# Kernel optimization log

Measured on AMD Instinct MI355X. Metric: run time of the kernel, lower is better.

Reference implementation:

```python
import jax, jax.numpy as jnp
import numpy as np

C_S, C_P, FEAT_DIM, NUM_BINS = 256, 128, 64, 22
MAX_DIST = 20.0
C_PAIR_PRE = 20
MAX_LEN = 2056.0


def get_index_embedding(indices, embed_size, max_len=MAX_LEN):
    # indices: (..., ) float; returns (..., embed_size) sinusoidal embedding
    K = jnp.arange(embed_size // 2, dtype=jnp.float32)
    ang = indices[..., None] * jnp.pi / (max_len ** (2.0 * K / embed_size))
    return jnp.concatenate([jnp.sin(ang), jnp.cos(ang)], axis=-1)


def rbf(D, D_min, D_max, D_count):
    # D: (...); returns (..., D_count) Gaussian RBF expansion
    D_mu = jnp.linspace(D_min, D_max, D_count)
    D_sigma = (D_max - D_min) / D_count
    return jnp.exp(-(((D[..., None] - D_mu) / D_sigma) ** 2))


def setup_inputs() -> dict:
    key = jax.random.key(0)
    ks = jax.random.split(key, 12)
    B, L = 1, 512
    total_edge = FEAT_DIM * 3 + NUM_BINS * 2 + C_PAIR_PRE  # 256
    inp = {
        "s": jax.random.normal(ks[0], (B, L, C_S), jnp.float32),
        "t": jax.random.normal(ks[1], (B, L, 3), jnp.float32),
        "sc_t": jax.random.normal(ks[2], (B, L, 3), jnp.float32),
        "pair_repr_pre": jax.random.normal(ks[3], (B, L, L, C_PAIR_PRE), jnp.float32),
        "p_mask": jnp.ones((B, L, L), jnp.float32),
        # linear_s_p: c_s -> feat_dim
        "W_sp": jax.random.normal(ks[4], (FEAT_DIM, C_S), jnp.float32) / np.sqrt(C_S),
        "b_sp": jnp.zeros((FEAT_DIM,), jnp.float32),
        # linear_relpos: feat_dim -> feat_dim
        "W_rp": jax.random.normal(ks[5], (FEAT_DIM, FEAT_DIM), jnp.float32) / np.sqrt(FEAT_DIM),
        "b_rp": jnp.zeros((FEAT_DIM,), jnp.float32),
        # edge_embedder: total_edge -> c_p -> c_p
        "W1": jax.random.normal(ks[6], (C_P, total_edge), jnp.float32) / np.sqrt(total_edge),
        "b1": jnp.zeros((C_P,), jnp.float32),
        "W2": jax.random.normal(ks[7], (C_P, C_P), jnp.float32) / np.sqrt(C_P),
        "b2": jnp.zeros((C_P,), jnp.float32),
    }
    return inp


def reference(s, t, sc_t, pair_repr_pre, p_mask, W_sp, b_sp, W_rp, b_rp, W1, b1, W2, b2):
    B, L, _ = s.shape
    # node projection then pairwise cross-concat -> (B, L, L, 2*feat_dim)
    p_i = jnp.einsum("bld,fd->blf", s, W_sp) + b_sp
    cross = jnp.concatenate([
        jnp.broadcast_to(p_i[:, :, None, :], (B, L, L, FEAT_DIM)),
        jnp.broadcast_to(p_i[:, None, :, :], (B, L, L, FEAT_DIM)),
    ], axis=-1)
    # relative-position sinusoidal embedding -> linear
    pos = jnp.arange(L, dtype=jnp.float32)[None, :]  # (1, L) broadcast over batch
    rel_pos = pos[:, :, None] - pos[:, None, :]      # (1, L, L)
    rel_pos = jnp.broadcast_to(rel_pos, (B, L, L))
    pos_emb = get_index_embedding(rel_pos, FEAT_DIM)
    relpos_feats = jnp.einsum("bijf,gf->bijg", pos_emb, W_rp) + b_rp
    # RBF distance expansions for backbone (t) and sidechain (sc_t) coords
    d_t = jnp.linalg.norm(t[:, :, None, :] - t[:, None, :, :], axis=-1)
    dist_feats = rbf(d_t, 0.0, MAX_DIST, NUM_BINS)
    d_sc = jnp.linalg.norm(sc_t[:, :, None, :] - sc_t[:, None, :, :], axis=-1)
    sc_feats = rbf(d_sc, 0.0, MAX_DIST, NUM_BINS)
    all_edge = jnp.concatenate([cross, relpos_feats, dist_feats, sc_feats, pair_repr_pre], axis=-1)
    # 2-layer MLP (dropout = 0 / eval mode)
    h = jax.nn.relu(jnp.einsum("bije,pe->bijp", all_edge, W1) + b1)
    edge_feats = jnp.einsum("bijp,qp->bijq", h, W2) + b2
    return edge_feats
```

## Files before the change

kernel.cpp:

```cpp
#include <hip/hip_runtime.h>
#include <hip/hip_bf16.h>


typedef __attribute__((ext_vector_type(8))) short v8s;
typedef __attribute__((ext_vector_type(4))) float v4f;

#define PI_F 3.14159265358979323846f

__device__ __forceinline__ unsigned short f2bu(float x) {
    __hip_bfloat16 h = __float2bfloat16(x);
    return *reinterpret_cast<unsigned short*>(&h);
}

__global__ __launch_bounds__(256) void precompute_kernel(
    const float* __restrict__ s, const float* __restrict__ W_sp,
    const float* __restrict__ b_sp, const float* __restrict__ W_rp,
    const float* __restrict__ b_rp, const float* __restrict__ W1,
    const float* __restrict__ W2,
    __hip_bfloat16* __restrict__ p_bf, __hip_bfloat16* __restrict__ relT,
    __hip_bfloat16* __restrict__ W1b, __hip_bfloat16* __restrict__ W2b)
{
    const int b = blockIdx.x;
    const int tid = threadIdx.x;
    __shared__ float lds[128 * 65 + 8 * 256];

    if (b < 64) {
        float* Wt   = lds;
        float* srow = lds + 128 * 65;
        const int row0 = b * 8;
        const int f  = tid & 63;
        const int rh = tid >> 6;
        #pragma unroll
        for (int k = 0; k < 8; k++) {
            const int idx = tid + 256 * k;
            const int r = idx >> 8, d = idx & 255;
            srow[r * 256 + d] = s[(row0 + r) * 256 + d];
        }
        float acc0 = b_sp[f];
        float acc1 = acc0;
        for (int pass = 0; pass < 2; pass++) {
            __syncthreads();
            #pragma unroll
            for (int k = 0; k < 32; k++) {
                const int idx = tid + 256 * k;
                const int fs = idx >> 7, ds = idx & 127;
                Wt[ds * 65 + fs] = W_sp[fs * 256 + pass * 128 + ds];
            }
            __syncthreads();
            #pragma unroll 4
            for (int d = 0; d < 128; d++) {
                const float w = Wt[d * 65 + f];
                acc0 += srow[rh * 256 + pass * 128 + d] * w;
                acc1 += srow[(rh + 4) * 256 + pass * 128 + d] * w;
            }
        }
        p_bf[(row0 + rh) * 64 + f]     = __float2bfloat16(acc0);
        p_bf[(row0 + rh + 4) * 64 + f] = __float2bfloat16(acc1);
    } else if (b < 320) {
        float* WrT  = lds;
        float* femb = lds + 64 * 65;
        const int r0 = (b - 64) * 4;
        #pragma unroll
        for (int k = 0; k < 16; k++) {
            const int idx = tid + 256 * k;
            const int g = idx >> 6, ff = idx & 63;
            WrT[ff * 65 + g] = W_rp[g * 64 + ff];
        }
        {
            const int r = tid >> 6, c = tid & 63;
            const float rel = (float)(r0 + r - 511);
            const int K = c & 31;
            const float freq = powf(2056.0f, (2.0f * (float)K) / 64.0f);
            const float ang = rel * PI_F / freq;
            femb[r * 64 + c] = (c < 32) ? sinf(ang) : cosf(ang);
        }
        __syncthreads();
        const int g = tid & 63, r = tid >> 6;
        float acc = b_rp[g];
        #pragma unroll
        for (int ff = 0; ff < 64; ff++) acc += femb[r * 64 + ff] * WrT[ff * 65 + g];
        relT[(r0 + r) * 64 + g] = __float2bfloat16(acc);
    } else {
        #pragma unroll
        for (int k = 0; k < 2; k++) {
            const int idx4 = (b - 320) * 512 + k * 256 + tid;
            const int e = idx4 * 4;
            const float4 v = (e < 32768) ? *(const float4*)&W1[e]
                                         : *(const float4*)&W2[e - 32768];
            __hip_bfloat16* dst = (e < 32768) ? (W1b + e) : (W2b + (e - 32768));
            dst[0] = __float2bfloat16(v.x);
            dst[1] = __float2bfloat16(v.y);
            dst[2] = __float2bfloat16(v.z);
            dst[3] = __float2bfloat16(v.w);
        }
    }
}

__global__ __launch_bounds__(256, 5) void edge_main(
    const float* __restrict__ t3, const float* __restrict__ sc3,
    const float* __restrict__ pre,
    const float* __restrict__ b1, const float* __restrict__ b2,
    const __hip_bfloat16* __restrict__ p_bf, const __hip_bfloat16* __restrict__ relT,
    const __hip_bfloat16* __restrict__ W1b, const __hip_bfloat16* __restrict__ W2b,
    float* __restrict__ out)
{
    __shared__ char smem[32768];

    const int tid = threadIdx.x;
    const int blk = blockIdx.x;
    const int i  = blk >> 3;
    const int j0 = (blk & 7) << 6;

    const int wv   = tid >> 6;
    const int lane = tid & 63;
    const int l16  = lane & 15;
    const int quad = lane >> 4;
    const int cbase = wv * 32;

    const float4 b1v0 = *(const float4*)&b1[cbase + quad * 4];
    const float4 b1v1 = *(const float4*)&b1[cbase + 16 + quad * 4];
    const float4 b2v0 = *(const float4*)&b2[cbase + quad * 4];
    const float4 b2v1 = *(const float4*)&b2[cbase + 16 + quad * 4];
    const __hip_bfloat16* w1m0 = W1b + (cbase + l16) * 256 + quad * 8;
    const __hip_bfloat16* w1m1 = w1m0 + 16 * 256;
    const __hip_bfloat16* w2m0 = W2b + (cbase + l16) * 128 + quad * 8;
    const __hip_bfloat16* w2m1 = w2m0 + 16 * 128;
    const v8s p10 = *(const v8s*)w1m0;
    const v8s p11 = *(const v8s*)w1m1;

    #pragma unroll
    for (int c = tid; c < 512; c += 256) {
        const int r  = c >> 3;
        const int ck = c & 7;
        const int px = (ck ^ (r & 7)) << 4;
        char* rowp = smem + r * 512;
        *(uint4*)(rowp + px)       = *(const uint4*)&p_bf[i * 64 + ck * 8];
        *(uint4*)(rowp + 128 + px) = *(const uint4*)&p_bf[(j0 + r) * 64 + ck * 8];
        *(uint4*)(rowp + 256 + px) = *(const uint4*)&relT[(i - (j0 + r) + 511) * 64 + ck * 8];
    }
    for (int c = tid; c < 320; c += 256) {
        const int r = c / 5;
        const int q = c % 5;
        const int col = 236 + q * 4;
        const float4 v = *(const float4*)&pre[((size_t)i * 512 + j0 + r) * 20 + q * 4];
        union { unsigned short s4[4]; uint2 u; } pk;
        pk.s4[0] = f2bu(v.x); pk.s4[1] = f2bu(v.y);
        pk.s4[2] = f2bu(v.z); pk.s4[3] = f2bu(v.w);
        const int off = r * 512 + (((col >> 3) ^ (r & 7)) << 4) + ((col & 7) * 2);
        *(uint2*)(smem + off) = pk.u;
    }
    {
        const int r  = tid >> 2;
        const int fo = (tid & 3) * 11;
        const int j = j0 + r;
        const float dxt = t3[i * 3 + 0] - t3[j * 3 + 0];
        const float dyt = t3[i * 3 + 1] - t3[j * 3 + 1];
        const float dzt = t3[i * 3 + 2] - t3[j * 3 + 2];
        const float dt = sqrtf(dxt * dxt + dyt * dyt + dzt * dzt);
        const float dxs = sc3[i * 3 + 0] - sc3[j * 3 + 0];
        const float dys = sc3[i * 3 + 1] - sc3[j * 3 + 1];
        const float dzs = sc3[i * 3 + 2] - sc3[j * 3 + 2];
        const float ds = sqrtf(dxs * dxs + dys * dys + dzs * dzs);
        char* rowp = smem + r * 512;
        const int rx = r & 7;
        #pragma unroll
        for (int q = 0; q < 11; q++) {
            const int f = fo + q;
            const float d = (f < 22) ? dt : ds;
            const int m = (f < 22) ? f : f - 22;
            const float x = (d - (float)m * (20.0f / 21.0f)) * 1.1f;
            const int col = 192 + f;
            const int off = (((col >> 3) ^ rx) << 4) + ((col & 7) * 2);
            *(unsigned short*)(rowp + off) = f2bu(__expf(-x * x));
        }
    }
    __syncthreads();

    const int xorv = (l16 & 7) << 4;
    v4f acc[2][4];
    #pragma unroll
    for (int mt = 0; mt < 2; mt++)
        #pragma unroll
        for (int nt = 0; nt < 4; nt++) acc[mt][nt] = (v4f){0.f, 0.f, 0.f, 0.f};

    #pragma unroll
    for (int kt = 0; kt < 8; kt++) {
        const int po = ((kt * 4 + quad) * 16) ^ xorv;
        const v8s t0 = *(const v8s*)(smem + (l16     ) * 512 + po);
        const v8s t1 = *(const v8s*)(smem + (l16 + 16) * 512 + po);
        const v8s t2 = *(const v8s*)(smem + (l16 + 32) * 512 + po);
        const v8s t3f = *(const v8s*)(smem + (l16 + 48) * 512 + po);
        const v8s w0 = (kt == 0) ? p10 : *(const v8s*)(w1m0 + kt * 32);
        const v8s w1f = (kt == 0) ? p11 : *(const v8s*)(w1m1 + kt * 32);
        acc[0][0] = __builtin_amdgcn_mfma_f32_16x16x32_bf16(w0, t0,  acc[0][0], 0, 0, 0);
        acc[0][1] = __builtin_amdgcn_mfma_f32_16x16x32_bf16(w0, t1,  acc[0][1], 0, 0, 0);
        acc[0][2] = __builtin_amdgcn_mfma_f32_16x16x32_bf16(w0, t2,  acc[0][2], 0, 0, 0);
        acc[0][3] = __builtin_amdgcn_mfma_f32_16x16x32_bf16(w0, t3f, acc[0][3], 0, 0, 0);
        acc[1][0] = __builtin_amdgcn_mfma_f32_16x16x32_bf16(w1f, t0,  acc[1][0], 0, 0, 0);
        acc[1][1] = __builtin_amdgcn_mfma_f32_16x16x32_bf16(w1f, t1,  acc[1][1], 0, 0, 0);
        acc[1][2] = __builtin_amdgcn_mfma_f32_16x16x32_bf16(w1f, t2,  acc[1][2], 0, 0, 0);
        acc[1][3] = __builtin_amdgcn_mfma_f32_16x16x32_bf16(w1f, t3f, acc[1][3], 0, 0, 0);
    }
    __syncthreads();

    #pragma unroll
    for (int mt = 0; mt < 2; mt++) {
        const float4 bv = mt ? b1v1 : b1v0;
        const int col = cbase + mt * 16 + quad * 4;
        #pragma unroll
        for (int nt = 0; nt < 4; nt++) {
            const int row = nt * 16 + l16;
            union { unsigned short s4[4]; uint2 u; } pk;
            pk.s4[0] = f2bu(fmaxf(acc[mt][nt][0] + bv.x, 0.f));
            pk.s4[1] = f2bu(fmaxf(acc[mt][nt][1] + bv.y, 0.f));
            pk.s4[2] = f2bu(fmaxf(acc[mt][nt][2] + bv.z, 0.f));
            pk.s4[3] = f2bu(fmaxf(acc[mt][nt][3] + bv.w, 0.f));
            const int off = row * 256 + (((col >> 3) ^ (row & 7)) << 4) + ((col & 7) * 2);
            *(uint2*)(smem + off) = pk.u;
        }
    }
    __syncthreads();

    v4f acc2[2][4];
    #pragma unroll
    for (int mt = 0; mt < 2; mt++)
        #pragma unroll
        for (int nt = 0; nt < 4; nt++) acc2[mt][nt] = (v4f){0.f, 0.f, 0.f, 0.f};

    #pragma unroll
    for (int kt = 0; kt < 4; kt++) {
        const int po = ((kt * 4 + quad) * 16) ^ xorv;
        const v8s t0 = *(const v8s*)(smem + (l16     ) * 256 + po);
        const v8s t1 = *(const v8s*)(smem + (l16 + 16) * 256 + po);
        const v8s t2 = *(const v8s*)(smem + (l16 + 32) * 256 + po);
        const v8s t3f = *(const v8s*)(smem + (l16 + 48) * 256 + po);
        const v8s w0 = *(const v8s*)(w2m0 + kt * 32);
        const v8s w1f = *(const v8s*)(w2m1 + kt * 32);
        acc2[0][0] = __builtin_amdgcn_mfma_f32_16x16x32_bf16(w0, t0,  acc2[0][0], 0, 0, 0);
        acc2[0][1] = __builtin_amdgcn_mfma_f32_16x16x32_bf16(w0, t1,  acc2[0][1], 0, 0, 0);
        acc2[0][2] = __builtin_amdgcn_mfma_f32_16x16x32_bf16(w0, t2,  acc2[0][2], 0, 0, 0);
        acc2[0][3] = __builtin_amdgcn_mfma_f32_16x16x32_bf16(w0, t3f, acc2[0][3], 0, 0, 0);
        acc2[1][0] = __builtin_amdgcn_mfma_f32_16x16x32_bf16(w1f, t0,  acc2[1][0], 0, 0, 0);
        acc2[1][1] = __builtin_amdgcn_mfma_f32_16x16x32_bf16(w1f, t1,  acc2[1][1], 0, 0, 0);
        acc2[1][2] = __builtin_amdgcn_mfma_f32_16x16x32_bf16(w1f, t2,  acc2[1][2], 0, 0, 0);
        acc2[1][3] = __builtin_amdgcn_mfma_f32_16x16x32_bf16(w1f, t3f, acc2[1][3], 0, 0, 0);
    }

    const size_t rowbase = (size_t)blk * 64;
    #pragma unroll
    for (int mt = 0; mt < 2; mt++) {
        const float4 bv = mt ? b2v1 : b2v0;
        const int col = cbase + mt * 16 + quad * 4;
        #pragma unroll
        for (int nt = 0; nt < 4; nt++) {
            const size_t row = rowbase + nt * 16 + l16;
            float4 o;
            o.x = acc2[mt][nt][0] + bv.x;
            o.y = acc2[mt][nt][1] + bv.y;
            o.z = acc2[mt][nt][2] + bv.z;
            o.w = acc2[mt][nt][3] + bv.w;
            *(float4*)&out[row * 128 + col] = o;
        }
    }
}

extern "C" void kernel_launch(void* const* d_in, const int* in_sizes, int n_in,
                              void* d_out, int out_size, void* d_ws, size_t ws_size,
                              hipStream_t stream) {
    const float* s    = (const float*)d_in[0];
    const float* t3   = (const float*)d_in[1];
    const float* sc3  = (const float*)d_in[2];
    const float* pre  = (const float*)d_in[3];
    const float* W_sp = (const float*)d_in[5];
    const float* b_sp = (const float*)d_in[6];
    const float* W_rp = (const float*)d_in[7];
    const float* b_rp = (const float*)d_in[8];
    const float* W1   = (const float*)d_in[9];
    const float* b1   = (const float*)d_in[10];
    const float* W2   = (const float*)d_in[11];
    const float* b2   = (const float*)d_in[12];
    float* out = (float*)d_out;

    char* ws = (char*)d_ws;
    __hip_bfloat16* p_bf = (__hip_bfloat16*)(ws);
    __hip_bfloat16* relT = (__hip_bfloat16*)(ws + 65536);
    __hip_bfloat16* W1b  = (__hip_bfloat16*)(ws + 65536 + 131072);
    __hip_bfloat16* W2b  = (__hip_bfloat16*)(ws + 65536 + 131072 + 65536);

    precompute_kernel<<<344, 256, 0, stream>>>(s, W_sp, b_sp, W_rp, b_rp, W1, W2,
                                               p_bf, relT, W1b, W2b);
    edge_main<<<4096, 256, 0, stream>>>(t3, sc3, pre, b1, b2,
                                        p_bf, relT, W1b, W2b, out);
}
```

Baseline: 227.3 us.

## Fold row-i projection into per-row bias and loop j-tiles with double buffering

Adds a small kernel that folds the p_i contribution through W1 into a per-row bias, which removes 64 of the 256 K columns from the first GEMM. The main kernel now runs one block per row i and loops over eight 64-column j tiles. W1 and W2 fragments stay in registers for the whole loop, and global loads for the next tile are issued before the current tile's MFMAs, with the tile built into a double-buffered LDS slot. The grid drops to 512 blocks with more registers and LDS per block, which lowers occupancy and parallelism and could leave CUs underused.

```diff
diff --git a/kernel.cpp b/kernel.cpp
--- a/kernel.cpp
+++ b/kernel.cpp
@@ -96,171 +96,225 @@
     }
 }
 
-__global__ __launch_bounds__(256, 5) void edge_main(
+__global__ __launch_bounds__(128) void bias1_kernel(
+    const __hip_bfloat16* __restrict__ p_bf, const __hip_bfloat16* __restrict__ W1b,
+    const float* __restrict__ b1, float* __restrict__ bias1)
+{
+    const int i = blockIdx.x;
+    const int c = threadIdx.x;
+    __shared__ float prow[64];
+    if (c < 64) prow[c] = __bfloat162float(p_bf[i * 64 + c]);
+    __syncthreads();
+    float acc = b1[c];
+    const __hip_bfloat16* w = W1b + c * 256;
+    #pragma unroll 8
+    for (int f = 0; f < 64; f++) acc += prow[f] * __bfloat162float(w[f]);
+    bias1[i * 128 + c] = acc;
+}
+
+__global__ __launch_bounds__(256, 2) void edge_main(
     const float* __restrict__ t3, const float* __restrict__ sc3,
-    const float* __restrict__ pre,
-    const float* __restrict__ b1, const float* __restrict__ b2,
+    const float* __restrict__ pre, const float* __restrict__ bias1,
+    const float* __restrict__ b2,
     const __hip_bfloat16* __restrict__ p_bf, const __hip_bfloat16* __restrict__ relT,
     const __hip_bfloat16* __restrict__ W1b, const __hip_bfloat16* __restrict__ W2b,
     float* __restrict__ out)
 {
-    __shared__ char smem[32768];
-
-    const int tid = threadIdx.x;
-    const int blk = blockIdx.x;
-    const int i  = blk >> 3;
-    const int j0 = (blk & 7) << 6;
-
+    __shared__ char smem[65536];
+
+    const int tid  = threadIdx.x;
+    const int i    = blockIdx.x;
     const int wv   = tid >> 6;
     const int lane = tid & 63;
     const int l16  = lane & 15;
     const int quad = lane >> 4;
     const int cbase = wv * 32;
-
-    const float4 b1v0 = *(const float4*)&b1[cbase + quad * 4];
-    const float4 b1v1 = *(const float4*)&b1[cbase + 16 + quad * 4];
-    const float4 b2v0 = *(const float4*)&b2[cbase + quad * 4];
-    const float4 b2v1 = *(const float4*)&b2[cbase + 16 + quad * 4];
-    const __hip_bfloat16* w1m0 = W1b + (cbase + l16) * 256 + quad * 8;
-    const __hip_bfloat16* w1m1 = w1m0 + 16 * 256;
-    const __hip_bfloat16* w2m0 = W2b + (cbase + l16) * 128 + quad * 8;
-    const __hip_bfloat16* w2m1 = w2m0 + 16 * 128;
-    const v8s p10 = *(const v8s*)w1m0;
-    const v8s p11 = *(const v8s*)w1m1;
-
-    #pragma unroll
-    for (int c = tid; c < 512; c += 256) {
-        const int r  = c >> 3;
-        const int ck = c & 7;
-        const int px = (ck ^ (r & 7)) << 4;
-        char* rowp = smem + r * 512;
-        *(uint4*)(rowp + px)       = *(const uint4*)&p_bf[i * 64 + ck * 8];
-        *(uint4*)(rowp + 128 + px) = *(const uint4*)&p_bf[(j0 + r) * 64 + ck * 8];
-        *(uint4*)(rowp + 256 + px) = *(const uint4*)&relT[(i - (j0 + r) + 511) * 64 + ck * 8];
+    const int rx16 = l16 & 7;
+
+    v8s w1f[2][6];
+    v8s w2f[2][4];
+    {
+        const __hip_bfloat16* a = W1b + (cbase + l16) * 256 + 64 + quad * 8;
+        #pragma unroll
+        for (int mt = 0; mt < 2; mt++)
+            #pragma unroll
+            for (int kt = 0; kt < 6; kt++)
+                w1f[mt][kt] = *(const v8s*)(a + mt * 16 * 256 + kt * 32);
+        const __hip_bfloat16* a2 = W2b + (cbase + l16) * 128 + quad * 8;
+        #pragma unroll
+        for (int mt = 0; mt < 2; mt++)
+            #pragma unroll
+            for (int kt = 0; kt < 4; kt++)
+                w2f[mt][kt] = *(const v8s*)(a2 + mt * 16 * 128 + kt * 32);
     }
-    for (int c = tid; c < 320; c += 256) {
-        const int r = c / 5;
-        const int q = c % 5;
-        const int col = 236 + q * 4;
-        const float4 v = *(const float4*)&pre[((size_t)i * 512 + j0 + r) * 20 + q * 4];
-        union { unsigned short s4[4]; uint2 u; } pk;
-        pk.s4[0] = f2bu(v.x); pk.s4[1] = f2bu(v.y);
-        pk.s4[2] = f2bu(v.z); pk.s4[3] = f2bu(v.w);
-        const int off = r * 512 + (((col >> 3) ^ (r & 7)) << 4) + ((col & 7) * 2);
-        *(uint2*)(smem + off) = pk.u;
-    }
-    {
-        const int r  = tid >> 2;
-        const int fo = (tid & 3) * 11;
-        const int j = j0 + r;
-        const float dxt = t3[i * 3 + 0] - t3[j * 3 + 0];
-        const float dyt = t3[i * 3 + 1] - t3[j * 3 + 1];
-        const float dzt = t3[i * 3 + 2] - t3[j * 3 + 2];
-        const float dt = sqrtf(dxt * dxt + dyt * dyt + dzt * dzt);
-        const float dxs = sc3[i * 3 + 0] - sc3[j * 3 + 0];
-        const float dys = sc3[i * 3 + 1] - sc3[j * 3 + 1];
-        const float dzs = sc3[i * 3 + 2] - sc3[j * 3 + 2];
-        const float ds = sqrtf(dxs * dxs + dys * dys + dzs * dzs);
-        char* rowp = smem + r * 512;
-        const int rx = r & 7;
-        #pragma unroll
-        for (int q = 0; q < 11; q++) {
-            const int f = fo + q;
-            const float d = (f < 22) ? dt : ds;
-            const int m = (f < 22) ? f : f - 22;
-            const float x = (d - (float)m * (20.0f / 21.0f)) * 1.1f;
-            const int col = 192 + f;
-            const int off = (((col >> 3) ^ rx) << 4) + ((col & 7) * 2);
-            *(unsigned short*)(rowp + off) = f2bu(__expf(-x * x));
-        }
-    }
+    const float4 bz0 = *(const float4*)&b2[cbase + quad * 4];
+    const float4 bz1 = *(const float4*)&b2[cbase + 16 + quad * 4];
+    const float4 bo0 = *(const float4*)&bias1[i * 128 + cbase + quad * 4];
+    const float4 bo1 = *(const float4*)&bias1[i * 128 + cbase + 16 + quad * 4];
+
+    const float tix = t3[i * 3], tiy = t3[i * 3 + 1], tiz = t3[i * 3 + 2];
+    const float six = sc3[i * 3], siy = sc3[i * 3 + 1], siz = sc3[i * 3 + 2];
+
+    const int rA = tid >> 3, ckA = tid & 7;
+    const int rB = rA + 32;
+    const int rp0 = tid / 5, qp0 = tid % 5;
+    const int rp1 = (tid + 256) / 5, qp1 = (tid + 256) % 5;
+    const int rr = tid >> 2, fo = (tid & 3) * 11;
+
+    uint4 s_pjA, s_pjB, s_rlA, s_rlB;
+    float4 s_prA, s_prB;
+    float s_dt, s_ds;
+
+    auto stage = [&](int j0n) {
+        s_pjA = *(const uint4*)&p_bf[(j0n + rA) * 64 + ckA * 8];
+        s_pjB = *(const uint4*)&p_bf[(j0n + rB) * 64 + ckA * 8];
+        s_rlA = *(const uint4*)&relT[(i - (j0n + rA) + 511) * 64 + ckA * 8];
+        s_rlB = *(const uint4*)&relT[(i - (j0n + rB) + 511) * 64 + ckA * 8];
+        s_prA = *(const float4*)&pre[((size_t)i * 512 + j0n + rp0) * 20 + qp0 * 4];
+        if (tid < 64)
+            s_prB = *(const float4*)&pre[((size_t)i * 512 + j0n + rp1) * 20 + qp1 * 4];
+        const int j = j0n + rr;
+        const float dx = tix - t3[j * 3], dy = tiy - t3[j * 3 + 1], dz = tiz - t3[j * 3 + 2];
+        s_dt = sqrtf(dx * dx + dy * dy + dz * dz);
+        const float ex = six - sc3[j * 3], ey = siy - sc3[j * 3 + 1], ez = siz - sc3[j * 3 + 2];
+        s_ds = sqrtf(ex * ex + ey * ey + ez * ez);
+    };
+
+    auto build = [&](char* T) {
+        {
+            const int xA = (ckA ^ (rA & 7)) << 4;
+            *(uint4*)(T + rA * 384 + xA)       = s_pjA;
+            *(uint4*)(T + rA * 384 + 128 + xA) = s_rlA;
+            const int xB = (ckA ^ (rB & 7)) << 4;
+            *(uint4*)(T + rB * 384 + xB)       = s_pjB;
+            *(uint4*)(T + rB * 384 + 128 + xB) = s_rlB;
+        }
+        {
+            union { unsigned short u2[4]; uint2 u; } pk;
+            const int sub0 = 44 + qp0 * 4;
+            pk.u2[0] = f2bu(s_prA.x); pk.u2[1] = f2bu(s_prA.y);
+            pk.u2[2] = f2bu(s_prA.z); pk.u2[3] = f2bu(s_prA.w);
+            *(uint2*)(T + rp0 * 384 + 256 + (((sub0 >> 3) ^ (rp0 & 7)) << 4) + (sub0 & 7) * 2) = pk.u;
+            if (tid < 64) {
+                const int sub1 = 44 + qp1 * 4;
+                pk.u2[0] = f2bu(s_prB.x); pk.u2[1] = f2bu(s_prB.y);
+                pk.u2[2] = f2bu(s_prB.z); pk.u2[3] = f2bu(s_prB.w);
+                *(uint2*)(T + rp1 * 384 + 256 + (((sub1 >> 3) ^ (rp1 & 7)) << 4) + (sub1 & 7) * 2) = pk.u;
+            }
+        }
+        {
+            const int rxr = rr & 7;
+            char* rowp = T + rr * 384 + 256;
+            #pragma unroll
+            for (int q = 0; q < 11; q++) {
+                const int f = fo + q;
+                const float d = (f < 22) ? s_dt : s_ds;
+                const int m = (f < 22) ? f : f - 22;
+                const float x = (d - (float)m * (20.0f / 21.0f)) * 1.1f;
+                *(unsigned short*)(rowp + (((f >> 3) ^ rxr) << 4) + (f & 7) * 2)
+                    = f2bu(__expf(-x * x));
+            }
+        }
+    };
+
+    stage(0);
+    build(smem);
     __syncthreads();
 
-    const int xorv = (l16 & 7) << 4;
-    v4f acc[2][4];
-    #pragma unroll
-    for (int mt = 0; mt < 2; mt++)
-        #pragma unroll
-        for (int nt = 0; nt < 4; nt++) acc[mt][nt] = (v4f){0.f, 0.f, 0.f, 0.f};
-
-    #pragma unroll
-    for (int kt = 0; kt < 8; kt++) {
-        const int po = ((kt * 4 + quad) * 16) ^ xorv;
-        const v8s t0 = *(const v8s*)(smem + (l16     ) * 512 + po);
-        const v8s t1 = *(const v8s*)(smem + (l16 + 16) * 512 + po);
-        const v8s t2 = *(const v8s*)(smem + (l16 + 32) * 512 + po);
-        const v8s t3f = *(const v8s*)(smem + (l16 + 48) * 512 + po);
-        const v8s w0 = (kt == 0) ? p10 : *(const v8s*)(w1m0 + kt * 32);
-        const v8s w1f = (kt == 0) ? p11 : *(const v8s*)(w1m1 + kt * 32);
-        acc[0][0] = __builtin_amdgcn_mfma_f32_16x16x32_bf16(w0, t0,  acc[0][0], 0, 0, 0);
-        acc[0][1] = __builtin_amdgcn_mfma_f32_16x16x32_bf16(w0, t1,  acc[0][1], 0, 0, 0);
-        acc[0][2] = __builtin_amdgcn_mfma_f32_16x16x32_bf16(w0, t2,  acc[0][2], 0, 0, 0);
-        acc[0][3] = __builtin_amdgcn_mfma_f32_16x16x32_bf16(w0, t3f, acc[0][3], 0, 0, 0);
-        acc[1][0] = __builtin_amdgcn_mfma_f32_16x16x32_bf16(w1f, t0,  acc[1][0], 0, 0, 0);
-        acc[1][1] = __builtin_amdgcn_mfma_f32_16x16x32_bf16(w1f, t1,  acc[1][1], 0, 0, 0);
-        acc[1][2] = __builtin_amdgcn_mfma_f32_16x16x32_bf16(w1f, t2,  acc[1][2], 0, 0, 0);
-        acc[1][3] = __builtin_amdgcn_mfma_f32_16x16x32_bf16(w1f, t3f, acc[1][3], 0, 0, 0);
-    }
-    __syncthreads();
-
-    #pragma unroll
-    for (int mt = 0; mt < 2; mt++) {
-        const float4 bv = mt ? b1v1 : b1v0;
-        const int col = cbase + mt * 16 + quad * 4;
-        #pragma unroll
-        for (int nt = 0; nt < 4; nt++) {
-            const int row = nt * 16 + l16;
-            union { unsigned short s4[4]; uint2 u; } pk;
-            pk.s4[0] = f2bu(fmaxf(acc[mt][nt][0] + bv.x, 0.f));
-            pk.s4[1] = f2bu(fmaxf(acc[mt][nt][1] + bv.y, 0.f));
-            pk.s4[2] = f2bu(fmaxf(acc[mt][nt][2] + bv.z, 0.f));
-            pk.s4[3] = f2bu(fmaxf(acc[mt][nt][3] + bv.w, 0.f));
-            const int off = row * 256 + (((col >> 3) ^ (row & 7)) << 4) + ((col & 7) * 2);
-            *(uint2*)(smem + off) = pk.u;
-        }
-    }
-    __syncthreads();
-
-    v4f acc2[2][4];
-    #pragma unroll
-    for (int mt = 0; mt < 2; mt++)
-        #pragma unroll
-        for (int nt = 0; nt < 4; nt++) acc2[mt][nt] = (v4f){0.f, 0.f, 0.f, 0.f};
-
-    #pragma unroll
-    for (int kt = 0; kt < 4; kt++) {
-        const int po = ((kt * 4 + quad) * 16) ^ xorv;
-        const v8s t0 = *(const v8s*)(smem + (l16     ) * 256 + po);
-        const v8s t1 = *(const v8s*)(smem + (l16 + 16) * 256 + po);
-        const v8s t2 = *(const v8s*)(smem + (l16 + 32) * 256 + po);
-        const v8s t3f = *(const v8s*)(smem + (l16 + 48) * 256 + po);
-        const v8s w0 = *(const v8s*)(w2m0 + kt * 32);
-        const v8s w1f = *(const v8s*)(w2m1 + kt * 32);
-        acc2[0][0] = __builtin_amdgcn_mfma_f32_16x16x32_bf16(w0, t0,  acc2[0][0], 0, 0, 0);
-        acc2[0][1] = __builtin_amdgcn_mfma_f32_16x16x32_bf16(w0, t1,  acc2[0][1], 0, 0, 0);
-        acc2[0][2] = __builtin_amdgcn_mfma_f32_16x16x32_bf16(w0, t2,  acc2[0][2], 0, 0, 0);
-        acc2[0][3] = __builtin_amdgcn_mfma_f32_16x16x32_bf16(w0, t3f, acc2[0][3], 0, 0, 0);
-        acc2[1][0] = __builtin_amdgcn_mfma_f32_16x16x32_bf16(w1f, t0,  acc2[1][0], 0, 0, 0);
-        acc2[1][1] = __builtin_amdgcn_mfma_f32_16x16x32_bf16(w1f, t1,  acc2[1][1], 0, 0, 0);
-        acc2[1][2] = __builtin_amdgcn_mfma_f32_16x16x32_bf16(w1f, t2,  acc2[1][2], 0, 0, 0);
-        acc2[1][3] = __builtin_amdgcn_mfma_f32_16x16x32_bf16(w1f, t3f, acc2[1][3], 0, 0, 0);
-    }
-
-    const size_t rowbase = (size_t)blk * 64;
-    #pragma unroll
-    for (int mt = 0; mt < 2; mt++) {
-        const float4 bv = mt ? b2v1 : b2v0;
-        const int col = cbase + mt * 16 + quad * 4;
-        #pragma unroll
-        for (int nt = 0; nt < 4; nt++) {
-            const size_t row = rowbase + nt * 16 + l16;
-            float4 o;
-            o.x = acc2[mt][nt][0] + bv.x;
-            o.y = acc2[mt][nt][1] + bv.y;
-            o.z = acc2[mt][nt][2] + bv.z;
-            o.w = acc2[mt][nt][3] + bv.w;
-            *(float4*)&out[row * 128 + col] = o;
-        }
+    char* Hb = smem + 49152;
+    const size_t orow0 = (size_t)i * 512;
+
+    #pragma unroll 1
+    for (int s = 0; s < 8; s++) {
+        char* T  = smem + ((s & 1) ? 24576 : 0);
+        char* Tn = smem + ((s & 1) ? 0 : 24576);
+        if (s < 7) stage((s + 1) * 64);
+
+        v4f acc[2][4];
+        #pragma unroll
+        for (int mt = 0; mt < 2; mt++)
+            #pragma unroll
+            for (int nt = 0; nt < 4; nt++) acc[mt][nt] = (v4f){0.f, 0.f, 0.f, 0.f};
+
+        #pragma unroll
+        for (int kt = 0; kt < 6; kt++) {
+            const int g = kt * 4 + quad;
+            const int po = ((g ^ rx16) << 4);
+            const v8s t0 = *(const v8s*)(T + (l16     ) * 384 + po);
+            const v8s t1 = *(const v8s*)(T + (l16 + 16) * 384 + po);
+            const v8s t2 = *(const v8s*)(T + (l16 + 32) * 384 + po);
+            const v8s t3v = *(const v8s*)(T + (l16 + 48) * 384 + po);
+            acc[0][0] = __builtin_amdgcn_mfma_f32_16x16x32_bf16(w1f[0][kt], t0,  acc[0][0], 0, 0, 0);
+            acc[0][1] = __builtin_amdgcn_mfma_f32_16x16x32_bf16(w1f[0][kt], t1,  acc[0][1], 0, 0, 0);
+            acc[0][2] = __builtin_amdgcn_mfma_f32_16x16x32_bf16(w1f[0][kt], t2,  acc[0][2], 0, 0, 0);
+            acc[0][3] = __builtin_amdgcn_mfma_f32_16x16x32_bf16(w1f[0][kt], t3v, acc[0][3], 0, 0, 0);
+            acc[1][0] = __builtin_amdgcn_mfma_f32_16x16x32_bf16(w1f[1][kt], t0,  acc[1][0], 0, 0, 0);
+            acc[1][1] = __builtin_amdgcn_mfma_f32_16x16x32_bf16(w1f[1][kt], t1,  acc[1][1], 0, 0, 0);
+            acc[1][2] = __builtin_amdgcn_mfma_f32_16x16x32_bf16(w1f[1][kt], t2,  acc[1][2], 0, 0, 0);
+            acc[1][3] = __builtin_amdgcn_mfma_f32_16x16x32_bf16(w1f[1][kt], t3v, acc[1][3], 0, 0, 0);
+        }
+
+        #pragma unroll
+        for (int mt = 0; mt < 2; mt++) {
+            const float4 bv = mt ? bo1 : bo0;
+            const int col = cbase + mt * 16 + quad * 4;
+            const int cch = col >> 3;
+            const int boff = (col & 7) * 2;
+            #pragma unroll
+            for (int nt = 0; nt < 4; nt++) {
+                const int row = nt * 16 + l16;
+                union { unsigned short u2[4]; uint2 u; } pk;
+                pk.u2[0] = f2bu(fmaxf(acc[mt][nt][0] + bv.x, 0.f));
+                pk.u2[1] = f2bu(fmaxf(acc[mt][nt][1] + bv.y, 0.f));
+                pk.u2[2] = f2bu(fmaxf(acc[mt][nt][2] + bv.z, 0.f));
+                pk.u2[3] = f2bu(fmaxf(acc[mt][nt][3] + bv.w, 0.f));
+                *(uint2*)(Hb + row * 256 + ((cch ^ (row & 7)) << 4) + boff) = pk.u;
+            }
+        }
+        __syncthreads();
+
+        v4f acc2[2][4];
+        #pragma unroll
+        for (int mt = 0; mt < 2; mt++)
+            #pragma unroll
+            for (int nt = 0; nt < 4; nt++) acc2[mt][nt] = (v4f){0.f, 0.f, 0.f, 0.f};
+
+        #pragma unroll
+        for (int kt = 0; kt < 4; kt++) {
+            const int g = kt * 4 + quad;
+            const int po = ((g ^ rx16) << 4);
+            const v8s t0 = *(const v8s*)(Hb + (l16     ) * 256 + po);
+            const v8s t1 = *(const v8s*)(Hb + (l16 + 16) * 256 + po);
+            const v8s t2 = *(const v8s*)(Hb + (l16 + 32) * 256 + po);
+            const v8s t3v = *(const v8s*)(Hb + (l16 + 48) * 256 + po);
+            acc2[0][0] = __builtin_amdgcn_mfma_f32_16x16x32_bf16(w2f[0][kt], t0,  acc2[0][0], 0, 0, 0);
+            acc2[0][1] = __builtin_amdgcn_mfma_f32_16x16x32_bf16(w2f[0][kt], t1,  acc2[0][1], 0, 0, 0);
+            acc2[0][2] = __builtin_amdgcn_mfma_f32_16x16x32_bf16(w2f[0][kt], t2,  acc2[0][2], 0, 0, 0);
+            acc2[0][3] = __builtin_amdgcn_mfma_f32_16x16x32_bf16(w2f[0][kt], t3v, acc2[0][3], 0, 0, 0);
+            acc2[1][0] = __builtin_amdgcn_mfma_f32_16x16x32_bf16(w2f[1][kt], t0,  acc2[1][0], 0, 0, 0);
+            acc2[1][1] = __builtin_amdgcn_mfma_f32_16x16x32_bf16(w2f[1][kt], t1,  acc2[1][1], 0, 0, 0);
+            acc2[1][2] = __builtin_amdgcn_mfma_f32_16x16x32_bf16(w2f[1][kt], t2,  acc2[1][2], 0, 0, 0);
+            acc2[1][3] = __builtin_amdgcn_mfma_f32_16x16x32_bf16(w2f[1][kt], t3v, acc2[1][3], 0, 0, 0);
+        }
+
+        #pragma unroll
+        for (int mt = 0; mt < 2; mt++) {
+            const float4 bv = mt ? bz1 : bz0;
+            const int col = cbase + mt * 16 + quad * 4;
+            #pragma unroll
+            for (int nt = 0; nt < 4; nt++) {
+                const size_t row = orow0 + s * 64 + nt * 16 + l16;
+                float4 o;
+                o.x = acc2[mt][nt][0] + bv.x;
+                o.y = acc2[mt][nt][1] + bv.y;
+                o.z = acc2[mt][nt][2] + bv.z;
+                o.w = acc2[mt][nt][3] + bv.w;
+                *(float4*)&out[row * 128 + col] = o;
+            }
+        }
+
+        if (s < 7) build(Tn);
+        __syncthreads();
     }
 }
 
@@ -284,11 +338,13 @@
     char* ws = (char*)d_ws;
     __hip_bfloat16* p_bf = (__hip_bfloat16*)(ws);
     __hip_bfloat16* relT = (__hip_bfloat16*)(ws + 65536);
-    __hip_bfloat16* W1b  = (__hip_bfloat16*)(ws + 65536 + 131072);
-    __hip_bfloat16* W2b  = (__hip_bfloat16*)(ws + 65536 + 131072 + 65536);
+    __hip_bfloat16* W1b  = (__hip_bfloat16*)(ws + 196608);
+    __hip_bfloat16* W2b  = (__hip_bfloat16*)(ws + 262144);
+    float*          bias1 = (float*)(ws + 294912);
 
     precompute_kernel<<<344, 256, 0, stream>>>(s, W_sp, b_sp, W_rp, b_rp, W1, W2,
                                                p_bf, relT, W1b, W2b);
-    edge_main<<<4096, 256, 0, stream>>>(t3, sc3, pre, b1, b2,
-                                        p_bf, relT, W1b, W2b, out);
-}
+    bias1_kernel<<<512, 128, 0, stream>>>(p_bf, W1b, b1, bias1);
+    edge_main<<<512, 256, 0, stream>>>(t3, sc3, pre, bias1, b2,
+                                       p_bf, relT, W1b, W2b, out);
+}
```

After: 200.6 us. 11.7% less time.
